# Optimization experiments

Hardware: AMD Instinct MI355X
Metric: run time of the kernel (lower is better)

## Reference

```python
import jax, jax.numpy as jnp
import numpy as np

N = 50000
E = 800000
IN_DIM = 128
HEADS = 4
OUT_DIM = 32
TOT = HEADS * OUT_DIM  # 128 == IN_DIM -> residual_proj is None
LN_EPS = 1e-5
NEG_SLOPE = 0.2


def setup_inputs() -> dict:
    key = jax.random.key(0)
    ks = jax.random.split(key, 10)
    x = jax.random.normal(ks[0], (N, IN_DIM), dtype=jnp.float32)
    # random edges guaranteed src != dst (PyG GATv2Conv removes then re-adds self loops)
    src = jax.random.randint(ks[1], (E,), 0, N)
    off = jax.random.randint(ks[2], (E,), 1, N)
    dst = (src + off) % N
    edge_index = jnp.stack([src, dst]).astype(jnp.int64)
    # glorot-style init for weights
    sc = 1.0 / np.sqrt(IN_DIM)
    W_l = jax.random.uniform(ks[3], (IN_DIM, TOT), jnp.float32, -sc, sc)
    b_l = jnp.zeros((TOT,), jnp.float32)
    W_r = jax.random.uniform(ks[4], (IN_DIM, TOT), jnp.float32, -sc, sc)
    b_r = jnp.zeros((TOT,), jnp.float32)
    att = jax.random.uniform(ks[5], (HEADS, OUT_DIM), jnp.float32, -sc, sc)
    bias = jnp.zeros((TOT,), jnp.float32)
    ln_g = jnp.ones((TOT,), jnp.float32)
    ln_b = jnp.zeros((TOT,), jnp.float32)
    return {"x": x, "edge_index": edge_index, "W_l": W_l, "b_l": b_l,
            "W_r": W_r, "b_r": b_r, "att": att, "bias": bias,
            "ln_g": ln_g, "ln_b": ln_b}


def _gatv2_layer(x, src, dst, W_l, b_l, W_r, b_r, att, bias, ln_g, ln_b):
    n = x.shape[0]
    # GATv2Conv: x_l = lin_l(x) (source/messages), x_r = lin_r(x) (target)
    xl = (x @ W_l + b_l).reshape(n, HEADS, OUT_DIM)
    xr = (x @ W_r + b_r).reshape(n, HEADS, OUT_DIM)
    m = xl[src] + xr[dst]                               # [E+N, H, D]
    s = jnp.einsum('ehd,hd->eh', jax.nn.leaky_relu(m, NEG_SLOPE), att)
    # per-destination softmax (every node has a self loop -> no empty segments)
    smax = jax.ops.segment_max(s, dst, num_segments=n)  # [N, H]
    e = jnp.exp(s - smax[dst])
    denom = jax.ops.segment_sum(e, dst, num_segments=n)
    alpha = e / denom[dst]                              # [E+N, H]
    out = jax.ops.segment_sum(alpha[..., None] * xl[src], dst, num_segments=n)
    out = out.reshape(n, TOT) + bias
    out = out + x                                       # residual (in_dim == total_out_dim)
    mu = jnp.mean(out, axis=-1, keepdims=True)
    var = jnp.mean(jnp.square(out - mu), axis=-1, keepdims=True)
    y = (out - mu) / jnp.sqrt(var + LN_EPS) * ln_g + ln_b
    return jax.nn.elu(y)


def reference(x, edge_index, W_l, b_l, W_r, b_r, att, bias, ln_g, ln_b):
    n = x.shape[0]
    loops = jnp.arange(n, dtype=edge_index.dtype)
    src = jnp.concatenate([edge_index[0], loops])
    dst = jnp.concatenate([edge_index[1], loops])
    return _gatv2_layer(x, src, dst, W_l, b_l, W_r, b_r, att, bias, ln_g, ln_b)
```

## Files before the change

kernel.cpp:

```cpp
#include <hip/hip_runtime.h>

#define N_NODES 50000
#define E_EDGES 800000
#define M_TOTAL (E_EDGES + N_NODES)
#define IN_DIM 128
#define HEADS 4
#define OUT_DIM 32
#define TOT 128
#define LN_EPS 1e-5f
#define NEG_SLOPE 0.2f
#define LOG2E 1.4426950408889634f

#define SCAN_NBLK ((N_NODES + 255) / 256)
#define GEMM_NBLK ((N_NODES + 63) / 64)
#define HIST_NBLK 64
#define EPB 13312
#define HEPB (EPB / 2)

typedef __bf16 bf16x8 __attribute__((ext_vector_type(8)));
typedef float  f32x4  __attribute__((ext_vector_type(4)));
typedef _Float16 h2   __attribute__((ext_vector_type(2)));

__device__ __forceinline__ float quad_sum(float p) {
    p += __int_as_float(__builtin_amdgcn_update_dpp(
        0, __float_as_int(p), 0xB1 , 0xF, 0xF, true));
    p += __int_as_float(__builtin_amdgcn_update_dpp(
        0, __float_as_int(p), 0x4E , 0xF, 0xF, true));
    return p;
}

__global__ __launch_bounds__(256) void wthist_kernel(
    const int* __restrict__ dsts,
    const float* __restrict__ Wl, const float* __restrict__ Wr,
    unsigned* __restrict__ WT, unsigned char* __restrict__ HP,
    unsigned char* __restrict__ rank8) {
    __shared__ unsigned cnt[N_NODES / 8];
    const int b = blockIdx.x, t = threadIdx.x;
    if (b < 64) {
        const int u = b * 256 + t;
        const int col = u >> 6, k2 = u & 63;
        const float* __restrict__ W = (col < 128) ? Wl : Wr;
        const int c = col & 127;
        union { __bf16 bb[2]; unsigned uu; } p;
        p.bb[0] = (__bf16)W[(2 * k2) * TOT + c];
        p.bb[1] = (__bf16)W[(2 * k2 + 1) * TOT + c];
        WT[col * 64 + k2] = p.uu;
        return;
    }
    const int hb = b - 64;
    const int m_begin = hb * EPB;
    const int m_end = min(m_begin + EPB, M_TOTAL);
    for (int i = t; i < N_NODES / 8; i += 256) cnt[i] = 0;
    __syncthreads();
    for (int m0 = m_begin + t * 4; m0 < m_end; m0 += 1024) {
        int d[4];
        if (m0 < E_EDGES) {
            const int4 dv = *(const int4*)&dsts[m0];
            d[0] = dv.x; d[1] = dv.y; d[2] = dv.z; d[3] = dv.w;
        } else {
            d[0] = m0 - E_EDGES; d[1] = d[0] + 1; d[2] = d[0] + 2; d[3] = d[0] + 3;
        }
        uchar4 r;
        unsigned old, sh;
        sh = (d[0] & 7) * 4; old = atomicAdd(&cnt[d[0] >> 3], 1u << sh);
        r.x = (unsigned char)((old >> sh) & 15u);
        sh = (d[1] & 7) * 4; old = atomicAdd(&cnt[d[1] >> 3], 1u << sh);
        r.y = (unsigned char)((old >> sh) & 15u);
        sh = (d[2] & 7) * 4; old = atomicAdd(&cnt[d[2] >> 3], 1u << sh);
        r.z = (unsigned char)((old >> sh) & 15u);
        sh = (d[3] & 7) * 4; old = atomicAdd(&cnt[d[3] >> 3], 1u << sh);
        r.w = (unsigned char)((old >> sh) & 15u);
        *(uchar4*)&rank8[m0] = r;
    }
    __syncthreads();
    unsigned* __restrict__ Hrow = (unsigned*)(HP + (size_t)hb * N_NODES);
    for (int i = t; i < N_NODES / 8; i += 256) {
        const unsigned w = cnt[i];
        const unsigned lo = (w & 15u) | (((w >> 4) & 15u) << 8) |
                            (((w >> 8) & 15u) << 16) | (((w >> 12) & 15u) << 24);
        const unsigned hi = ((w >> 16) & 15u) | (((w >> 20) & 15u) << 8) |
                            (((w >> 24) & 15u) << 16) | (((w >> 28) & 15u) << 24);
        *(uint2*)&Hrow[2 * i] = make_uint2(lo, hi);
    }
}

__global__ __launch_bounds__(256) void gemm_kernel(
    const float* __restrict__ x, const unsigned* __restrict__ WT,
    const float* __restrict__ bl, const float* __restrict__ br,
    unsigned* __restrict__ xlb, unsigned* __restrict__ xrb) {
    __shared__ float epi[4][16][66];
    __shared__ unsigned Bs[64][68];
    const int t = threadIdx.x, w = t >> 6, lane = t & 63;
    const int q = lane >> 4, ln = lane & 15;
    const int m0 = blockIdx.x * 64;

    const int row = min(m0 + w * 16 + ln, N_NODES - 1);
    const float* __restrict__ xrow = x + (size_t)row * IN_DIM;
    bf16x8 A[4];
#pragma unroll
    for (int c = 0; c < 4; ++c) {
        const float4 v0 = *(const float4*)&xrow[c * 32 + q * 8];
        const float4 v1 = *(const float4*)&xrow[c * 32 + q * 8 + 4];
        bf16x8 a;
        a[0] = (__bf16)v0.x; a[1] = (__bf16)v0.y; a[2] = (__bf16)v0.z; a[3] = (__bf16)v0.w;
        a[4] = (__bf16)v1.x; a[5] = (__bf16)v1.y; a[6] = (__bf16)v1.z; a[7] = (__bf16)v1.w;
        A[c] = a;
    }

    const int mr = lane >> 2, cg2 = (lane & 3) * 16;
    const int grow = m0 + w * 16 + mr;
#pragma unroll
    for (int g = 0; g < 4; ++g) {
        const int n0 = g * 64;
        __syncthreads();
        {
            const unsigned* __restrict__ src = WT + n0 * 64;
#pragma unroll
            for (int it = 0; it < 4; ++it) {
                const int dw = t * 4 + it * 1024;
                const uint4 v = *(const uint4*)&src[dw];
                *(uint4*)&Bs[dw >> 6][dw & 63] = v;
            }
        }
        __syncthreads();
        const float* __restrict__ bvec = (g < 2) ? bl : br;
        f32x4 acc[4];
#pragma unroll
        for (int nt = 0; nt < 4; ++nt) {
            const float b = bvec[(n0 & 127) + nt * 16 + ln];
            acc[nt] = (f32x4){b, b, b, b};
        }
#pragma unroll
        for (int nt = 0; nt < 4; ++nt) {
#pragma unroll
            for (int c = 0; c < 4; ++c) {
                const bf16x8 B = *(const bf16x8*)&Bs[nt * 16 + ln][c * 16 + q * 4];
                acc[nt] = __builtin_amdgcn_mfma_f32_16x16x32_bf16(A[c], B, acc[nt], 0, 0, 0);
            }
        }
#pragma unroll
        for (int nt = 0; nt < 4; ++nt)
#pragma unroll
            for (int r = 0; r < 4; ++r)
                epi[w][q * 4 + r][nt * 16 + ln] = acc[nt][r];

        if (grow < N_NODES) {
            unsigned p[8];
#pragma unroll
            for (int i = 0; i < 8; ++i) {
                union { _Float16 h[2]; unsigned u; } pk;
                pk.h[0] = (_Float16)epi[w][mr][cg2 + 2 * i];
                pk.h[1] = (_Float16)epi[w][mr][cg2 + 2 * i + 1];
                p[i] = pk.u;
            }
            unsigned* __restrict__ dst = ((g < 2) ? xlb : xrb) +
                (size_t)grow * 64 + (g & 1) * 32 + (cg2 >> 1);
            *(uint4*)&dst[0] = make_uint4(p[0], p[1], p[2], p[3]);
            *(uint4*)&dst[4] = make_uint4(p[4], p[5], p[6], p[7]);
        }
    }
}

__global__ __launch_bounds__(256) void scan1_kernel(
    unsigned char* __restrict__ HP,
    int* __restrict__ rowptr, int* __restrict__ blockSums) {
    __shared__ int sh[256];
    const int t = threadIdx.x;
    const int i = blockIdx.x * 256 + t;
    int tot = 0;
    if (i < N_NODES) {
        int run = 0;
#pragma unroll 16
        for (int b = 0; b < HIST_NBLK; ++b) {
            const int h = HP[(size_t)b * N_NODES + i];
            HP[(size_t)b * N_NODES + i] = (unsigned char)run;
            run += h;
        }
        tot = run;
    }
    sh[t] = tot;
    __syncthreads();
#pragma unroll
    for (int off = 1; off < 256; off <<= 1) {
        int u = (t >= off) ? sh[t - off] : 0;
        __syncthreads();
        sh[t] += u;
        __syncthreads();
    }
    if (i < N_NODES) rowptr[i] = sh[t] - tot;
    if (t == 255) blockSums[blockIdx.x] = sh[255];
}

__global__ __launch_bounds__(256) void scan23_kernel(
    const int* __restrict__ blockSums,
    int* __restrict__ rowptr ,
    unsigned short* __restrict__ sorted16) {
    __shared__ int sh[256];
    const int t = threadIdx.x;
    const int v0 = (t < SCAN_NBLK) ? blockSums[t] : 0;
    sh[t] = v0;
    __syncthreads();
#pragma unroll
    for (int off = 1; off < 256; off <<= 1) {
        int u = (t >= off) ? sh[t - off] : 0;
        __syncthreads();
        sh[t] += u;
        __syncthreads();
    }
    const int blockOff = (blockIdx.x == 0) ? 0 : sh[blockIdx.x - 1];
    const int i = blockIdx.x * 256 + t;
    if (i < N_NODES) rowptr[i] += blockOff;
    if (i == 0) rowptr[N_NODES] = M_TOTAL;
    if (blockIdx.x == 0 && t < 32) sorted16[M_TOTAL + t] = 0;
}

__global__ __launch_bounds__(1024) void scatter_kernel(
    const int* __restrict__ srcs, const int* __restrict__ dsts,
    const int* __restrict__ rowptr, const unsigned char* __restrict__ P,
    const unsigned char* __restrict__ rank8,
    unsigned short* __restrict__ sorted16) {
    __shared__ __align__(16) unsigned char smem[N_NODES];
    const int t = threadIdx.x;
    const int sb = blockIdx.x;
    const int hb = sb >> 1;
    const uint4* __restrict__ Prow = (const uint4*)(P + (size_t)hb * N_NODES);
    for (int i = t; i < N_NODES / 16; i += 1024)
        ((uint4*)smem)[i] = Prow[i];
    __syncthreads();
    const int eb = hb * EPB + (sb & 1) * HEPB;
    const int ee = min(eb + HEPB, M_TOTAL);
    for (int m0 = eb + t * 4; m0 < ee; m0 += 4096) {
        int s[4], d[4];
        if (m0 < E_EDGES) {
            const int4 sv = *(const int4*)&srcs[m0];
            const int4 dv = *(const int4*)&dsts[m0];
            s[0] = sv.x; s[1] = sv.y; s[2] = sv.z; s[3] = sv.w;
            d[0] = dv.x; d[1] = dv.y; d[2] = dv.z; d[3] = dv.w;
        } else {
            s[0] = d[0] = m0 - E_EDGES;
            s[1] = d[1] = d[0] + 1; s[2] = d[2] = d[0] + 2; s[3] = d[3] = d[0] + 3;
        }
        const uchar4 r = *(const uchar4*)&rank8[m0];
        sorted16[rowptr[d[0]] + (int)smem[d[0]] + (int)r.x] = (unsigned short)s[0];
        sorted16[rowptr[d[1]] + (int)smem[d[1]] + (int)r.y] = (unsigned short)s[1];
        sorted16[rowptr[d[2]] + (int)smem[d[2]] + (int)r.z] = (unsigned short)s[2];
        sorted16[rowptr[d[3]] + (int)smem[d[3]] + (int)r.w] = (unsigned short)s[3];
    }
}

__global__ __launch_bounds__(256) void gat_kernel(
    const int* __restrict__ rowptr, const unsigned short* __restrict__ sorted16,
    const unsigned* __restrict__ xlb, const unsigned* __restrict__ xrb,
    const float* __restrict__ att, const float* __restrict__ x,
    const float* __restrict__ bias, const float* __restrict__ g,
    const float* __restrict__ bvec, float* __restrict__ out) {
    const int d = blockIdx.x * 4 + (threadIdx.x >> 6);
    const int lane = threadIdx.x & 63;
    const int ln = lane & 15, q = lane >> 4;
    if (d >= N_NODES) return;

    h2 xrh[4], ath[4];
    {
        const uint4 ur = *(const uint4*)&xrb[(size_t)d * 64 + 4 * ln];
        union { uint4 u; h2 h[4]; } cr; cr.u = ur;
        xrh[0] = cr.h[0]; xrh[1] = cr.h[1]; xrh[2] = cr.h[2]; xrh[3] = cr.h[3];
        const float4 a0 = *(const float4*)&att[8 * ln];
        const float4 a1 = *(const float4*)&att[8 * ln + 4];
        ath[0][0] = (_Float16)(a0.x * LOG2E); ath[0][1] = (_Float16)(a0.y * LOG2E);
        ath[1][0] = (_Float16)(a0.z * LOG2E); ath[1][1] = (_Float16)(a0.w * LOG2E);
        ath[2][0] = (_Float16)(a1.x * LOG2E); ath[2][1] = (_Float16)(a1.y * LOG2E);
        ath[3][0] = (_Float16)(a1.z * LOG2E); ath[3][1] = (_Float16)(a1.w * LOG2E);
    }
    const h2 slope = (h2){(_Float16)NEG_SLOPE, (_Float16)NEG_SLOPE};
    const int beg = rowptr[d], end = rowptr[d + 1];

    float l = 0.f;
    h2 acc4[4];
#pragma unroll
    for (int k = 0; k < 4; ++k) acc4[k] = (h2){(_Float16)0.f, (_Float16)0.f};

    uint4 u0, u1;
    {
        const int sA0 = (int)sorted16[min(beg + q, end - 1)];
        const int sA1 = (int)sorted16[min(beg + 4 + q, end - 1)];
        u0 = *(const uint4*)&xlb[(size_t)sA0 * 64 + 4 * ln];
        u1 = *(const uint4*)&xlb[(size_t)sA1 * 64 + 4 * ln];
    }
    int sB0 = (int)sorted16[min(beg + 8 + q, end - 1)];
    int sB1 = (int)sorted16[min(beg + 12 + q, end - 1)];

    for (int base = beg; base < end; base += 8) {
        const int sC0 = (int)sorted16[min(base + 16 + q, end - 1)];
        const int sC1 = (int)sorted16[min(base + 20 + q, end - 1)];
        const uint4 un0 = *(const uint4*)&xlb[(size_t)sB0 * 64 + 4 * ln];
        const uint4 un1 = *(const uint4*)&xlb[(size_t)sB1 * 64 + 4 * ln];

        union { unsigned uu; h2 h; } a0, a1, a2, a3, b0, b1, b2, b3;
        a0.uu = u0.x; a1.uu = u0.y; a2.uu = u0.z; a3.uu = u0.w;
        b0.uu = u1.x; b1.uu = u1.y; b2.uu = u1.z; b3.uu = u1.w;
        h2 mA0 = a0.h + xrh[0], mA1 = a1.h + xrh[1];
        h2 mA2 = a2.h + xrh[2], mA3 = a3.h + xrh[3];
        h2 mB0 = b0.h + xrh[0], mB1 = b1.h + xrh[1];
        h2 mB2 = b2.h + xrh[2], mB3 = b3.h + xrh[3];
        mA0 = __builtin_elementwise_max(mA0, mA0 * slope);
        mA1 = __builtin_elementwise_max(mA1, mA1 * slope);
        mA2 = __builtin_elementwise_max(mA2, mA2 * slope);
        mA3 = __builtin_elementwise_max(mA3, mA3 * slope);
        mB0 = __builtin_elementwise_max(mB0, mB0 * slope);
        mB1 = __builtin_elementwise_max(mB1, mB1 * slope);
        mB2 = __builtin_elementwise_max(mB2, mB2 * slope);
        mB3 = __builtin_elementwise_max(mB3, mB3 * slope);
        float p0 = __builtin_amdgcn_fdot2(mA0, ath[0], 0.0f, false);
        p0 = __builtin_amdgcn_fdot2(mA1, ath[1], p0, false);
        p0 = __builtin_amdgcn_fdot2(mA2, ath[2], p0, false);
        p0 = __builtin_amdgcn_fdot2(mA3, ath[3], p0, false);
        float p1 = __builtin_amdgcn_fdot2(mB0, ath[0], 0.0f, false);
        p1 = __builtin_amdgcn_fdot2(mB1, ath[1], p1, false);
        p1 = __builtin_amdgcn_fdot2(mB2, ath[2], p1, false);
        p1 = __builtin_amdgcn_fdot2(mB3, ath[3], p1, false);
        p0 = quad_sum(p0);
        p1 = quad_sum(p1);
        const float e0 = (base + q < end) ? exp2f(p0) : 0.f;
        const float e1 = (base + 4 + q < end) ? exp2f(p1) : 0.f;
        l += e0 + e1;
        const _Float16 eh0 = (_Float16)e0, eh1 = (_Float16)e1;
        const h2 e20 = (h2){eh0, eh0}, e21 = (h2){eh1, eh1};
        acc4[0] += e20 * a0.h; acc4[0] += e21 * b0.h;
        acc4[1] += e20 * a1.h; acc4[1] += e21 * b1.h;
        acc4[2] += e20 * a2.h; acc4[2] += e21 * b2.h;
        acc4[3] += e20 * a3.h; acc4[3] += e21 * b3.h;

        u0 = un0; u1 = un1; sB0 = sC0; sB1 = sC1;
    }

#pragma unroll
    for (int off = 16; off <= 32; off <<= 1) {
        l += __shfl_xor(l, off, 64);
#pragma unroll
        for (int k = 0; k < 4; ++k) {
            union { h2 h; int i; } tmp; tmp.h = acc4[k];
            tmp.i = __shfl_xor(tmp.i, off, 64);
            acc4[k] += tmp.h;
        }
    }
    float acc[8];
#pragma unroll
    for (int k = 0; k < 4; ++k) {
        acc[2 * k]     = (float)acc4[k][0];
        acc[2 * k + 1] = (float)acc4[k][1];
    }

    const float inv_l = 1.0f / l;
    const float4 xv0 = *(const float4*)&x[(size_t)d * TOT + 8 * ln];
    const float4 xv1 = *(const float4*)&x[(size_t)d * TOT + 8 * ln + 4];
    const float4 bi0 = *(const float4*)&bias[8 * ln];
    const float4 bi1 = *(const float4*)&bias[8 * ln + 4];
    float v[8];
    v[0] = fmaf(acc[0], inv_l, bi0.x + xv0.x);
    v[1] = fmaf(acc[1], inv_l, bi0.y + xv0.y);
    v[2] = fmaf(acc[2], inv_l, bi0.z + xv0.z);
    v[3] = fmaf(acc[3], inv_l, bi0.w + xv0.w);
    v[4] = fmaf(acc[4], inv_l, bi1.x + xv1.x);
    v[5] = fmaf(acc[5], inv_l, bi1.y + xv1.y);
    v[6] = fmaf(acc[6], inv_l, bi1.z + xv1.z);
    v[7] = fmaf(acc[7], inv_l, bi1.w + xv1.w);
    float sum = 0.f, sq = 0.f;
#pragma unroll
    for (int k = 0; k < 8; ++k) { sum += v[k]; sq = fmaf(v[k], v[k], sq); }
#pragma unroll
    for (int off = 1; off <= 8; off <<= 1) {
        sum += __shfl_xor(sum, off, 64);
        sq  += __shfl_xor(sq,  off, 64);
    }
    const float mu  = sum * (1.0f / TOT);
    const float var = sq * (1.0f / TOT) - mu * mu;
    const float inv = rsqrtf(var + LN_EPS);
    const float4 g0 = *(const float4*)&g[8 * ln];
    const float4 g1 = *(const float4*)&g[8 * ln + 4];
    const float4 b0 = *(const float4*)&bvec[8 * ln];
    const float4 b1 = *(const float4*)&bvec[8 * ln + 4];
    float y[8];
    y[0] = (v[0] - mu) * inv * g0.x + b0.x;
    y[1] = (v[1] - mu) * inv * g0.y + b0.y;
    y[2] = (v[2] - mu) * inv * g0.z + b0.z;
    y[3] = (v[3] - mu) * inv * g0.w + b0.w;
    y[4] = (v[4] - mu) * inv * g1.x + b1.x;
    y[5] = (v[5] - mu) * inv * g1.y + b1.y;
    y[6] = (v[6] - mu) * inv * g1.z + b1.z;
    y[7] = (v[7] - mu) * inv * g1.w + b1.w;
#pragma unroll
    for (int k = 0; k < 8; ++k) y[k] = y[k] > 0.f ? y[k] : __expf(y[k]) - 1.f;
    if (q < 2) {
        float4 o = (q == 0) ? make_float4(y[0], y[1], y[2], y[3])
                            : make_float4(y[4], y[5], y[6], y[7]);
        *(float4*)&out[(size_t)d * TOT + 8 * ln + 4 * q] = o;
    }
}

extern "C" void kernel_launch(void* const* d_in, const int* in_sizes, int n_in,
                              void* d_out, int out_size, void* d_ws, size_t ws_size,
                              hipStream_t stream) {
    const float* x    = (const float*)d_in[0];
    const int*   ei   = (const int*)d_in[1];
    const float* Wl   = (const float*)d_in[2];
    const float* bl   = (const float*)d_in[3];
    const float* Wr   = (const float*)d_in[4];
    const float* br   = (const float*)d_in[5];
    const float* att  = (const float*)d_in[6];
    const float* bias = (const float*)d_in[7];
    const float* ln_g = (const float*)d_in[8];
    const float* ln_b = (const float*)d_in[9];
    const int* srcs = ei;
    const int* dsts = ei + E_EDGES;

    unsigned* xlb = (unsigned*)d_ws;
    unsigned* xrb = xlb + (size_t)N_NODES * 64;
    int*   rowptr     = (int*)(xrb + (size_t)N_NODES * 64);
    int*   blockSums  = rowptr + N_NODES + 1;
    unsigned* WT      = (unsigned*)(blockSums + SCAN_NBLK + 4);
    unsigned char* HP = (unsigned char*)(WT + 256 * 64);
    unsigned short* sorted16 = (unsigned short*)(HP + (size_t)HIST_NBLK * N_NODES);
    unsigned char*  rank8    = (unsigned char*)(sorted16 + M_TOTAL + 32);

    wthist_kernel<<<64 + HIST_NBLK, 256, 0, stream>>>(dsts, Wl, Wr, WT, HP, rank8);
    gemm_kernel<<<GEMM_NBLK, 256, 0, stream>>>(x, WT, bl, br, xlb, xrb);
    scan1_kernel<<<SCAN_NBLK, 256, 0, stream>>>(HP, rowptr, blockSums);
    scan23_kernel<<<SCAN_NBLK, 256, 0, stream>>>(blockSums, rowptr, sorted16);
    scatter_kernel<<<2 * HIST_NBLK, 1024, 0, stream>>>(srcs, dsts, rowptr, HP, rank8, sorted16);
    gat_kernel<<<(N_NODES + 3) / 4, 256, 0, stream>>>(rowptr, sorted16, xlb, xrb, att, x,
                                                      bias, ln_g, ln_b, (float*)d_out);
}
```

Before: 173.4 us.

## Fuse GEMM and edge scatter into one launch with finer scatter blocks

Merges the projection GEMM and the CSR scatter into a single kernel, with block index choosing the role, so both run concurrently after the scan and one launch is saved. The scatter now reads per-block histogram offsets straight from global memory instead of staging a 50KB LDS copy, and uses 8 smaller 256-thread blocks per histogram chunk instead of 2 large 1024-thread blocks. This trades LDS staging for scattered global byte reads, and the GEMM no longer overlaps with the scan kernels.

New measurement: 172.0 us. About the same (-0.8%).

```diff
diff --git a/kernel.cpp b/kernel.cpp
--- a/kernel.cpp
+++ b/kernel.cpp
@@ -15,7 +15,8 @@
 #define GEMM_NBLK ((N_NODES + 63) / 64)
 #define HIST_NBLK 64
 #define EPB 13312
-#define HEPB (EPB / 2)
+#define SEPB (EPB / 8)
+#define SCAT_NBLK (HIST_NBLK * 8)
 
 typedef __bf16 bf16x8 __attribute__((ext_vector_type(8)));
 typedef float  f32x4  __attribute__((ext_vector_type(4)));
@@ -84,83 +85,6 @@
     }
 }
 
-__global__ __launch_bounds__(256) void gemm_kernel(
-    const float* __restrict__ x, const unsigned* __restrict__ WT,
-    const float* __restrict__ bl, const float* __restrict__ br,
-    unsigned* __restrict__ xlb, unsigned* __restrict__ xrb) {
-    __shared__ float epi[4][16][66];
-    __shared__ unsigned Bs[64][68];
-    const int t = threadIdx.x, w = t >> 6, lane = t & 63;
-    const int q = lane >> 4, ln = lane & 15;
-    const int m0 = blockIdx.x * 64;
-
-    const int row = min(m0 + w * 16 + ln, N_NODES - 1);
-    const float* __restrict__ xrow = x + (size_t)row * IN_DIM;
-    bf16x8 A[4];
-#pragma unroll
-    for (int c = 0; c < 4; ++c) {
-        const float4 v0 = *(const float4*)&xrow[c * 32 + q * 8];
-        const float4 v1 = *(const float4*)&xrow[c * 32 + q * 8 + 4];
-        bf16x8 a;
-        a[0] = (__bf16)v0.x; a[1] = (__bf16)v0.y; a[2] = (__bf16)v0.z; a[3] = (__bf16)v0.w;
-        a[4] = (__bf16)v1.x; a[5] = (__bf16)v1.y; a[6] = (__bf16)v1.z; a[7] = (__bf16)v1.w;
-        A[c] = a;
-    }
-
-    const int mr = lane >> 2, cg2 = (lane & 3) * 16;
-    const int grow = m0 + w * 16 + mr;
-#pragma unroll
-    for (int g = 0; g < 4; ++g) {
-        const int n0 = g * 64;
-        __syncthreads();
-        {
-            const unsigned* __restrict__ src = WT + n0 * 64;
-#pragma unroll
-            for (int it = 0; it < 4; ++it) {
-                const int dw = t * 4 + it * 1024;
-                const uint4 v = *(const uint4*)&src[dw];
-                *(uint4*)&Bs[dw >> 6][dw & 63] = v;
-            }
-        }
-        __syncthreads();
-        const float* __restrict__ bvec = (g < 2) ? bl : br;
-        f32x4 acc[4];
-#pragma unroll
-        for (int nt = 0; nt < 4; ++nt) {
-            const float b = bvec[(n0 & 127) + nt * 16 + ln];
-            acc[nt] = (f32x4){b, b, b, b};
-        }
-#pragma unroll
-        for (int nt = 0; nt < 4; ++nt) {
-#pragma unroll
-            for (int c = 0; c < 4; ++c) {
-                const bf16x8 B = *(const bf16x8*)&Bs[nt * 16 + ln][c * 16 + q * 4];
-                acc[nt] = __builtin_amdgcn_mfma_f32_16x16x32_bf16(A[c], B, acc[nt], 0, 0, 0);
-            }
-        }
-#pragma unroll
-        for (int nt = 0; nt < 4; ++nt)
-#pragma unroll
-            for (int r = 0; r < 4; ++r)
-                epi[w][q * 4 + r][nt * 16 + ln] = acc[nt][r];
-
-        if (grow < N_NODES) {
-            unsigned p[8];
-#pragma unroll
-            for (int i = 0; i < 8; ++i) {
-                union { _Float16 h[2]; unsigned u; } pk;
-                pk.h[0] = (_Float16)epi[w][mr][cg2 + 2 * i];
-                pk.h[1] = (_Float16)epi[w][mr][cg2 + 2 * i + 1];
-                p[i] = pk.u;
-            }
-            unsigned* __restrict__ dst = ((g < 2) ? xlb : xrb) +
-                (size_t)grow * 64 + (g & 1) * 32 + (cg2 >> 1);
-            *(uint4*)&dst[0] = make_uint4(p[0], p[1], p[2], p[3]);
-            *(uint4*)&dst[4] = make_uint4(p[4], p[5], p[6], p[7]);
-        }
-    }
-}
-
 __global__ __launch_bounds__(256) void scan1_kernel(
     unsigned char* __restrict__ HP,
     int* __restrict__ rowptr, int* __restrict__ blockSums) {
@@ -214,37 +138,110 @@
     if (blockIdx.x == 0 && t < 32) sorted16[M_TOTAL + t] = 0;
 }
 
-__global__ __launch_bounds__(1024) void scatter_kernel(
+__global__ __launch_bounds__(256) void gemmscatter_kernel(
+    const float* __restrict__ x, const unsigned* __restrict__ WT,
+    const float* __restrict__ bl, const float* __restrict__ br,
+    unsigned* __restrict__ xlb, unsigned* __restrict__ xrb,
     const int* __restrict__ srcs, const int* __restrict__ dsts,
     const int* __restrict__ rowptr, const unsigned char* __restrict__ P,
     const unsigned char* __restrict__ rank8,
     unsigned short* __restrict__ sorted16) {
-    __shared__ __align__(16) unsigned char smem[N_NODES];
+    __shared__ float epi[4][16][66];
+    __shared__ unsigned Bs[64][68];
     const int t = threadIdx.x;
-    const int sb = blockIdx.x;
-    const int hb = sb >> 1;
-    const uint4* __restrict__ Prow = (const uint4*)(P + (size_t)hb * N_NODES);
-    for (int i = t; i < N_NODES / 16; i += 1024)
-        ((uint4*)smem)[i] = Prow[i];
-    __syncthreads();
-    const int eb = hb * EPB + (sb & 1) * HEPB;
-    const int ee = min(eb + HEPB, M_TOTAL);
-    for (int m0 = eb + t * 4; m0 < ee; m0 += 4096) {
-        int s[4], d[4];
-        if (m0 < E_EDGES) {
-            const int4 sv = *(const int4*)&srcs[m0];
-            const int4 dv = *(const int4*)&dsts[m0];
-            s[0] = sv.x; s[1] = sv.y; s[2] = sv.z; s[3] = sv.w;
-            d[0] = dv.x; d[1] = dv.y; d[2] = dv.z; d[3] = dv.w;
-        } else {
-            s[0] = d[0] = m0 - E_EDGES;
-            s[1] = d[1] = d[0] + 1; s[2] = d[2] = d[0] + 2; s[3] = d[3] = d[0] + 3;
-        }
-        const uchar4 r = *(const uchar4*)&rank8[m0];
-        sorted16[rowptr[d[0]] + (int)smem[d[0]] + (int)r.x] = (unsigned short)s[0];
-        sorted16[rowptr[d[1]] + (int)smem[d[1]] + (int)r.y] = (unsigned short)s[1];
-        sorted16[rowptr[d[2]] + (int)smem[d[2]] + (int)r.z] = (unsigned short)s[2];
-        sorted16[rowptr[d[3]] + (int)smem[d[3]] + (int)r.w] = (unsigned short)s[3];
+    if (blockIdx.x >= GEMM_NBLK) {
+        const int sb = blockIdx.x - GEMM_NBLK;
+        const int hb = sb >> 3;
+        const unsigned char* __restrict__ Pb = P + (size_t)hb * N_NODES;
+        const int eb = hb * EPB + (sb & 7) * SEPB;
+        const int ee = min(eb + SEPB, M_TOTAL);
+        for (int m0 = eb + t * 4; m0 < ee; m0 += 1024) {
+            int s[4], d[4];
+            if (m0 < E_EDGES) {
+                const int4 sv = *(const int4*)&srcs[m0];
+                const int4 dv = *(const int4*)&dsts[m0];
+                s[0] = sv.x; s[1] = sv.y; s[2] = sv.z; s[3] = sv.w;
+                d[0] = dv.x; d[1] = dv.y; d[2] = dv.z; d[3] = dv.w;
+            } else {
+                s[0] = d[0] = m0 - E_EDGES;
+                s[1] = d[1] = d[0] + 1; s[2] = d[2] = d[0] + 2; s[3] = d[3] = d[0] + 3;
+            }
+            const uchar4 r = *(const uchar4*)&rank8[m0];
+            sorted16[rowptr[d[0]] + (int)Pb[d[0]] + (int)r.x] = (unsigned short)s[0];
+            sorted16[rowptr[d[1]] + (int)Pb[d[1]] + (int)r.y] = (unsigned short)s[1];
+            sorted16[rowptr[d[2]] + (int)Pb[d[2]] + (int)r.z] = (unsigned short)s[2];
+            sorted16[rowptr[d[3]] + (int)Pb[d[3]] + (int)r.w] = (unsigned short)s[3];
+        }
+        return;
+    }
+    const int w = t >> 6, lane = t & 63;
+    const int q = lane >> 4, ln = lane & 15;
+    const int m0 = blockIdx.x * 64;
+
+    const int row = min(m0 + w * 16 + ln, N_NODES - 1);
+    const float* __restrict__ xrow = x + (size_t)row * IN_DIM;
+    bf16x8 A[4];
+#pragma unroll
+    for (int c = 0; c < 4; ++c) {
+        const float4 v0 = *(const float4*)&xrow[c * 32 + q * 8];
+        const float4 v1 = *(const float4*)&xrow[c * 32 + q * 8 + 4];
+        bf16x8 a;
+        a[0] = (__bf16)v0.x; a[1] = (__bf16)v0.y; a[2] = (__bf16)v0.z; a[3] = (__bf16)v0.w;
+        a[4] = (__bf16)v1.x; a[5] = (__bf16)v1.y; a[6] = (__bf16)v1.z; a[7] = (__bf16)v1.w;
+        A[c] = a;
+    }
+
+    const int mr = lane >> 2, cg2 = (lane & 3) * 16;
+    const int grow = m0 + w * 16 + mr;
+#pragma unroll
+    for (int g = 0; g < 4; ++g) {
+        const int n0 = g * 64;
+        __syncthreads();
+        {
+            const unsigned* __restrict__ src = WT + n0 * 64;
+#pragma unroll
+            for (int it = 0; it < 4; ++it) {
+                const int dw = t * 4 + it * 1024;
+                const uint4 v = *(const uint4*)&src[dw];
+                *(uint4*)&Bs[dw >> 6][dw & 63] = v;
+            }
+        }
+        __syncthreads();
+        const float* __restrict__ bvec = (g < 2) ? bl : br;
+        f32x4 acc[4];
+#pragma unroll
+        for (int nt = 0; nt < 4; ++nt) {
+            const float b = bvec[(n0 & 127) + nt * 16 + ln];
+            acc[nt] = (f32x4){b, b, b, b};
+        }
+#pragma unroll
+        for (int nt = 0; nt < 4; ++nt) {
+#pragma unroll
+            for (int c = 0; c < 4; ++c) {
+                const bf16x8 B = *(const bf16x8*)&Bs[nt * 16 + ln][c * 16 + q * 4];
+                acc[nt] = __builtin_amdgcn_mfma_f32_16x16x32_bf16(A[c], B, acc[nt], 0, 0, 0);
+            }
+        }
+#pragma unroll
+        for (int nt = 0; nt < 4; ++nt)
+#pragma unroll
+            for (int r = 0; r < 4; ++r)
+                epi[w][q * 4 + r][nt * 16 + ln] = acc[nt][r];
+
+        if (grow < N_NODES) {
+            unsigned p[8];
+#pragma unroll
+            for (int i = 0; i < 8; ++i) {
+                union { _Float16 h[2]; unsigned u; } pk;
+                pk.h[0] = (_Float16)epi[w][mr][cg2 + 2 * i];
+                pk.h[1] = (_Float16)epi[w][mr][cg2 + 2 * i + 1];
+                p[i] = pk.u;
+            }
+            unsigned* __restrict__ dst = ((g < 2) ? xlb : xrb) +
+                (size_t)grow * 64 + (g & 1) * 32 + (cg2 >> 1);
+            *(uint4*)&dst[0] = make_uint4(p[0], p[1], p[2], p[3]);
+            *(uint4*)&dst[4] = make_uint4(p[4], p[5], p[6], p[7]);
+        }
     }
 }
 
@@ -423,10 +420,10 @@
     unsigned char*  rank8    = (unsigned char*)(sorted16 + M_TOTAL + 32);
 
     wthist_kernel<<<64 + HIST_NBLK, 256, 0, stream>>>(dsts, Wl, Wr, WT, HP, rank8);
-    gemm_kernel<<<GEMM_NBLK, 256, 0, stream>>>(x, WT, bl, br, xlb, xrb);
     scan1_kernel<<<SCAN_NBLK, 256, 0, stream>>>(HP, rowptr, blockSums);
     scan23_kernel<<<SCAN_NBLK, 256, 0, stream>>>(blockSums, rowptr, sorted16);
-    scatter_kernel<<<2 * HIST_NBLK, 1024, 0, stream>>>(srcs, dsts, rowptr, HP, rank8, sorted16);
+    gemmscatter_kernel<<<GEMM_NBLK + SCAT_NBLK, 256, 0, stream>>>(
+        x, WT, bl, br, xlb, xrb, srcs, dsts, rowptr, HP, rank8, sorted16);
     gat_kernel<<<(N_NODES + 3) / 4, 256, 0, stream>>>(rowptr, sorted16, xlb, xrb, att, x,
                                                       bias, ln_g, ln_b, (float*)d_out);
 }
```
